# Optimization experiments

Hardware: AMD Instinct MI355X
Metric: run time of the kernel (lower is better)

## Reference

```python
import jax, jax.numpy as jnp
import numpy as np

T_ITERS = 48  # number of unrolled PDHG iterations (init kwarg T)


def _grad3(u):
    """Forward-difference gradient with circular BC.
    u: (P, 1, X, Y, T) -> (P, 3, X, Y, T).
    conv with kernel (0,-1,1) + circular pad == roll(v,-1,axis) - v."""
    v = u[:, 0]
    return jnp.stack([jnp.roll(v, -1, axis=a) - v for a in (1, 2, 3)], axis=1)


def _grad3_adj(q):
    """Adjoint (negative divergence) with circular BC.
    q: (P, 3, X, Y, T) -> (P, 1, X, Y, T)."""
    out = sum(jnp.roll(q[:, d], 1, axis=d + 1) - q[:, d] for d in range(3))
    return out[:, None]


def setup_inputs() -> dict:
    key = jax.random.key(0)
    k1, k2 = jax.random.split(key)
    x = jax.random.normal(k1, (2, 1, 160, 160, 16), dtype=jnp.float32)
    # positive per-voxel regularization map, one per gradient direction
    lambda_map = jax.random.uniform(k2, (2, 3, 160, 160, 16), dtype=jnp.float32)
    return {"x": x, "lambda_map": lambda_map}


def reference(x, lambda_map):
    # op_norm_AHA = 1, op_norm_GHG = sqrt(12) -> L = sqrt(1 + 12)
    L = jnp.sqrt(jnp.asarray(13.0, x.dtype))
    s10 = jax.nn.sigmoid(jnp.asarray(10.0, x.dtype))  # sigmoid of init value 10.0
    sigma = s10 / L
    tau = s10 / L
    theta = s10

    xnoisy = x
    p = x
    q = jnp.zeros((x.shape[0], 3) + x.shape[2:], dtype=x.dtype)
    x0 = x
    xbar = x

    def step(carry, _):
        p, q, x0, xbar = carry
        p = (p + sigma * (xbar - xnoisy)) / (1.0 + sigma)
        q = jnp.clip(q + sigma * _grad3(xbar), -lambda_map, lambda_map)
        x1 = x0 - tau * p - tau * _grad3_adj(q)
        xbar = x1 + theta * (x1 - x0)
        return (p, q, x1, xbar), None

    (p, q, x1, xbar), _ = jax.lax.scan(step, (p, q, x0, xbar), None, length=T_ITERS)
    return x1
```

## Files before the change

kernel.cpp:

```cpp
#include <hip/hip_runtime.h>
#include <math.h>

#define XDIM 160
#define YDIM 160
#define TDIM 16
#define NB 2
#define T_ITERS 48
#define TILE 10
#define R1S 16
#define R0S 18
#define TPT (XDIM / TILE)

constexpr int VOL  = XDIM * YDIM * TDIM;
constexpr int NX   = NB * VOL;
constexpr int NBLK = NB * TPT * TPT;

typedef _Float16 hreal;
typedef _Float16 half4 __attribute__((ext_vector_type(4)));

__device__ __forceinline__ float clampl(float v, float l) {
    return fminf(fmaxf(v, -l), l);
}
__device__ __forceinline__ int wrap(int v) {
    return v < 0 ? v + XDIM : (v >= XDIM ? v - XDIM : v);
}
__device__ __forceinline__ void ld4(const float* p, float* d) {
    float4 v = *(const float4*)p;
    d[0] = v.x; d[1] = v.y; d[2] = v.z; d[3] = v.w;
}
__device__ __forceinline__ void st4(float* p, const float* s) {
    *(float4*)p = make_float4(s[0], s[1], s[2], s[3]);
}
__device__ __forceinline__ void h2f4(const hreal* p, float* d) {
    half4 v = *(const half4*)p;
    d[0] = (float)v.x; d[1] = (float)v.y; d[2] = (float)v.z; d[3] = (float)v.w;
}

__global__ __launch_bounds__(256) void init_kernel(
    const float* __restrict__ x, const float* __restrict__ lam,
    float* __restrict__ pA, float* __restrict__ xA,
    hreal* __restrict__ xbAh, hreal* __restrict__ qAh,
    hreal* __restrict__ lamh, hreal* __restrict__ xnh)
{
    int i = blockIdx.x * blockDim.x + threadIdx.x;
    if (i < NX) {
        float v = x[i];
        pA[i] = v; xA[i] = v;
        xbAh[i] = (hreal)v;
        xnh[i]  = (hreal)v;
    }
    if (i < 3 * NX) {
        qAh[i]  = (hreal)0.f;
        lamh[i] = (hreal)lam[i];
    }
}

__global__ __launch_bounds__(256, 2) void pd_step4(
    const hreal* __restrict__ xnh, const hreal* __restrict__ lamh,
    const float* __restrict__ pIn, float* __restrict__ pOut,
    const float* __restrict__ xIn, float* __restrict__ xOut,
    const hreal* __restrict__ xbIn, hreal* __restrict__ xbOut,
    const hreal* __restrict__ qIn, hreal* __restrict__ qOut,
    float sigma, float inv1ps, float tau, float theta)
{
    __shared__ float xbS[R0S * R0S * TDIM];
    __shared__ float q0S[(R1S + 1) * R1S * TDIM];
    __shared__ float q1S[R1S * (R1S + 1) * TDIM];

    const int tid = threadIdx.x;
    const int b   = blockIdx.x / (TPT * TPT);
    const int rem = blockIdx.x % (TPT * TPT);
    const int X0  = (rem / TPT) * TILE;
    const int Y0  = (rem % TPT) * TILE;
    const int xbase = b * VOL, qbase = b * 3 * VOL;

    const int qd = tid & 3, t0 = qd * 4;
    const int lane  = tid & 63;
    const int upSrc = (lane & 60) | ((lane + 1) & 3);
    const int dnSrc = (lane & 60) | ((lane + 3) & 3);

    for (int s = tid; s < R0S * R0S * 4; s += 256) {
        int sq = s & 3, ln = s >> 2;
        int rx = ln / R0S, ry = ln % R0S;
        int gx = wrap(X0 - 4 + rx), gy = wrap(Y0 - 4 + ry);
        float v[4];
        h2f4(xbIn + xbase + (gx * YDIM + gy) * TDIM + sq * 4, v);
        st4(xbS + ln * TDIM + sq * 4, v);
    }
    for (int s = tid; s < 17 * 16 * 4; s += 256) {
        int sq = s & 3, ln = s >> 2;
        int sx = ln / 16, sy = ln % 16;
        int gx = wrap(X0 - 4 + sx), gy = wrap(Y0 - 3 + sy);
        float v[4];
        h2f4(qIn + qbase + (gx * YDIM + gy) * TDIM + sq * 4, v);
        st4(q0S + ln * TDIM + sq * 4, v);
    }
    for (int s = tid; s < 16 * 17 * 4; s += 256) {
        int sq = s & 3, ln = s >> 2;
        int sx = ln / 17, sy = ln % 17;
        int gx = wrap(X0 - 3 + sx), gy = wrap(Y0 - 4 + sy);
        float v[4];
        h2f4(qIn + qbase + VOL + (gx * YDIM + gy) * TDIM + sq * 4, v);
        st4(q1S + ln * TDIM + sq * 4, v);
    }

    float p[4][4], xv[4][4], xb[4][4], q0[4][4], q1[4][4], q2[4][4];
    half4 XNr[4], L0r[4], L1r[4], L2r[4];
    #pragma unroll
    for (int m = 0; m < 4; ++m) {
        int line = 64 * m + (tid >> 2);
        int lx = line >> 4, ly = line & 15;
        int gx = wrap(X0 - 3 + lx), gy = wrap(Y0 - 3 + ly);
        int off  = xbase + (gx * YDIM + gy) * TDIM + t0;
        int qoff = qbase + (gx * YDIM + gy) * TDIM + t0;
        ld4(pIn + off, p[m]);
        ld4(xIn + off, xv[m]);
        h2f4(xbIn + off, xb[m]);
        h2f4(qIn + qoff + 2 * VOL, q2[m]);
        XNr[m] = *(const half4*)(xnh + off);
        L0r[m] = *(const half4*)(lamh + qoff);
        L1r[m] = *(const half4*)(lamh + qoff + VOL);
        L2r[m] = *(const half4*)(lamh + qoff + 2 * VOL);
    }

    half4 LRr;
    if (tid < 64) {
        int rly = tid >> 2;
        LRr = *(const half4*)(lamh + qbase +
              (wrap(X0 - 4) * YDIM + wrap(Y0 - 3 + rly)) * TDIM + t0);
    } else if (tid < 128) {
        int rlx = (tid - 64) >> 2;
        LRr = *(const half4*)(lamh + qbase + VOL +
              (wrap(X0 - 3 + rlx) * YDIM + wrap(Y0 - 4)) * TDIM + t0);
    }

    __syncthreads();

    #pragma unroll
    for (int k = 1; k <= 4; ++k) {
        const int lo = k - 1, hi = 17 - k;

        if (k == 1) {
            if (tid < 64) {
                int rly = tid >> 2;
                float qr[4], xbc[4], xpx[4];
                ld4(q0S + (0 * R1S + rly) * TDIM + t0, qr);
                ld4(xbS + (0 * R0S + (rly + 1)) * TDIM + t0, xbc);
                ld4(xbS + (1 * R0S + (rly + 1)) * TDIM + t0, xpx);
                #pragma unroll
                for (int j = 0; j < 4; ++j)
                    qr[j] = clampl(qr[j] + sigma * (xpx[j] - xbc[j]), (float)LRr[j]);
                st4(q0S + (0 * R1S + rly) * TDIM + t0, qr);
            } else if (tid < 128) {
                int rlx = (tid - 64) >> 2;
                float qr[4], xbc[4], xpy[4];
                ld4(q1S + (rlx * 17 + 0) * TDIM + t0, qr);
                ld4(xbS + ((rlx + 1) * R0S + 0) * TDIM + t0, xbc);
                ld4(xbS + ((rlx + 1) * R0S + 1) * TDIM + t0, xpy);
                #pragma unroll
                for (int j = 0; j < 4; ++j)
                    qr[j] = clampl(qr[j] + sigma * (xpy[j] - xbc[j]), (float)LRr[j]);
                st4(q1S + (rlx * 17 + 0) * TDIM + t0, qr);
            }
        }

        #pragma unroll
        for (int m = 0; m < 4; ++m) {
            int line = 64 * m + (tid >> 2);
            int lx = line >> 4, ly = line & 15;
            bool inX = (lx >= lo && lx < hi), inY = (ly >= lo && ly < hi);
            bool aq0 = inY && (lx >= lo - 1) && (lx < hi);
            bool aq1 = inX && (ly >= lo - 1) && (ly < hi);
            bool ax  = inX && inY;

            if (k == 1) {
                ld4(q0S + ((lx + 1) * R1S + ly) * TDIM + t0, q0[m]);
                ld4(q1S + (lx * 17 + (ly + 1)) * TDIM + t0, q1[m]);
            }
            if (aq0) {
                float xpx[4];
                ld4(xbS + ((lx + 2) * R0S + (ly + 1)) * TDIM + t0, xpx);
                #pragma unroll
                for (int j = 0; j < 4; ++j)
                    q0[m][j] = clampl(q0[m][j] + sigma * (xpx[j] - xb[m][j]),
                                      (float)L0r[m][j]);
                st4(q0S + ((lx + 1) * R1S + ly) * TDIM + t0, q0[m]);
            }
            if (aq1) {
                float xpy[4];
                ld4(xbS + ((lx + 1) * R0S + (ly + 2)) * TDIM + t0, xpy);
                #pragma unroll
                for (int j = 0; j < 4; ++j)
                    q1[m][j] = clampl(q1[m][j] + sigma * (xpy[j] - xb[m][j]),
                                      (float)L1r[m][j]);
                st4(q1S + (lx * 17 + (ly + 1)) * TDIM + t0, q1[m]);
            }
            if (ax) {
                float xb_tp = __shfl(xb[m][0], upSrc, 64);
                #pragma unroll
                for (int j = 0; j < 4; ++j) {
                    float gt = ((j < 3) ? xb[m][j + 1] : xb_tp) - xb[m][j];
                    q2[m][j] = clampl(q2[m][j] + sigma * gt, (float)L2r[m][j]);
                    p[m][j]  = (p[m][j] + sigma * (xb[m][j] - (float)XNr[m][j]))
                               * inv1ps;
                }
            }
        }
        __syncthreads();

        #pragma unroll
        for (int m = 0; m < 4; ++m) {
            int line = 64 * m + (tid >> 2);
            int lx = line >> 4, ly = line & 15;
            bool ax = (lx >= lo && lx < hi && ly >= lo && ly < hi);
            if (ax) {
                float q0b[4], q1b[4];
                ld4(q0S + (lx * R1S + ly) * TDIM + t0, q0b);
                ld4(q1S + (lx * 17 + ly) * TDIM + t0, q1b);
                float q2tm = __shfl(q2[m][3], dnSrc, 64);
                #pragma unroll
                for (int j = 0; j < 4; ++j) {
                    float q2p = (j == 0) ? q2tm : q2[m][j - 1];
                    float div = (q0b[j] - q0[m][j]) + (q1b[j] - q1[m][j])
                              + (q2p - q2[m][j]);
                    float xnew = xv[m][j] - tau * (p[m][j] + div);
                    xb[m][j] = xnew + theta * (xnew - xv[m][j]);
                    xv[m][j] = xnew;
                }
                if (k < 4)
                    st4(xbS + ((lx + 1) * R0S + (ly + 1)) * TDIM + t0, xb[m]);
            }
        }
        if (k < 4) __syncthreads();
    }

    #pragma unroll
    for (int m = 0; m < 4; ++m) {
        int line = 64 * m + (tid >> 2);
        int lx = line >> 4, ly = line & 15;
        if (lx >= 3 && lx < 13 && ly >= 3 && ly < 13) {
            int gx = X0 + lx - 3, gy = Y0 + ly - 3;
            int off  = xbase + (gx * YDIM + gy) * TDIM + t0;
            int qoff = qbase + (gx * YDIM + gy) * TDIM + t0;
            st4(pOut + off, p[m]);
            st4(xOut + off, xv[m]);
            half4 h;
            h.x = (hreal)xb[m][0]; h.y = (hreal)xb[m][1];
            h.z = (hreal)xb[m][2]; h.w = (hreal)xb[m][3];
            *(half4*)(xbOut + off) = h;
            h.x = (hreal)q0[m][0]; h.y = (hreal)q0[m][1];
            h.z = (hreal)q0[m][2]; h.w = (hreal)q0[m][3];
            *(half4*)(qOut + qoff) = h;
            h.x = (hreal)q1[m][0]; h.y = (hreal)q1[m][1];
            h.z = (hreal)q1[m][2]; h.w = (hreal)q1[m][3];
            *(half4*)(qOut + qoff + VOL) = h;
            h.x = (hreal)q2[m][0]; h.y = (hreal)q2[m][1];
            h.z = (hreal)q2[m][2]; h.w = (hreal)q2[m][3];
            *(half4*)(qOut + qoff + 2 * VOL) = h;
        }
    }
}

extern "C" void kernel_launch(void* const* d_in, const int* in_sizes, int n_in,
                              void* d_out, int out_size, void* d_ws, size_t ws_size,
                              hipStream_t stream) {
    const float* x   = (const float*)d_in[0];
    const float* lam = (const float*)d_in[1];
    float* out = (float*)d_out;
    float* ws  = (float*)d_ws;

    float* pA  = ws;
    float* pB  = ws + (size_t)NX;
    float* xBb = ws + (size_t)2 * NX;
    float* xAb = out;
    hreal* hb  = (hreal*)(ws + (size_t)3 * NX);
    hreal* xbAh = hb;
    hreal* xbBh = hb + (size_t)NX;
    hreal* qAh  = hb + (size_t)2 * NX;
    hreal* qBh  = hb + (size_t)5 * NX;
    hreal* lamh = hb + (size_t)8 * NX;
    hreal* xnh  = hb + (size_t)11 * NX;

    const double s10 = 1.0 / (1.0 + exp(-10.0));
    const double L   = sqrt(13.0);
    float sigma  = (float)(s10 / L);
    float tau    = sigma;
    float theta  = (float)s10;
    float inv1ps = (float)(1.0 / (1.0 + s10 / L));

    init_kernel<<<(3 * NX + 255) / 256, 256, 0, stream>>>(
        x, lam, pA, xAb, xbAh, qAh, lamh, xnh);

    for (int j = 0; j < T_ITERS / 4; ++j) {
        const bool e = (j & 1) == 0;
        pd_step4<<<NBLK, 256, 0, stream>>>(
            xnh, lamh,
            e ? pA : pB,   e ? pB : pA,
            e ? xAb : xBb, e ? xBb : xAb,
            e ? xbAh : xbBh, e ? xbBh : xbAh,
            e ? qAh : qBh,  e ? qBh : qAh,
            sigma, inv1ps, tau, theta);
    }
}
```

Before: 298.3 us.

## Fuse eight PDHG iterations per launch with fp16 shared-memory tiles

```diff
diff --git a/kernel.cpp b/kernel.cpp
--- a/kernel.cpp
+++ b/kernel.cpp
@@ -7,9 +7,12 @@
 #define NB 2
 #define T_ITERS 48
 #define TILE 10
-#define R1S 16
-#define R0S 18
+#define KFUSE 8
+#define S1 24
+#define S0 26
 #define TPT (XDIM / TILE)
+#define NTHR 512
+#define NSLOT 5
 
 constexpr int VOL  = XDIM * YDIM * TDIM;
 constexpr int NX   = NB * VOL;
@@ -34,6 +37,11 @@
 __device__ __forceinline__ void h2f4(const hreal* p, float* d) {
     half4 v = *(const half4*)p;
     d[0] = (float)v.x; d[1] = (float)v.y; d[2] = (float)v.z; d[3] = (float)v.w;
+}
+__device__ __forceinline__ void f2h4(hreal* p, const float* s) {
+    half4 v;
+    v.x = (hreal)s[0]; v.y = (hreal)s[1]; v.z = (hreal)s[2]; v.w = (hreal)s[3];
+    *(half4*)p = v;
 }
 
 __global__ __launch_bounds__(256) void init_kernel(
@@ -55,7 +63,7 @@
     }
 }
 
-__global__ __launch_bounds__(256, 2) void pd_step4(
+__global__ __launch_bounds__(NTHR, 4) void pd_step8(
     const hreal* __restrict__ xnh, const hreal* __restrict__ lamh,
     const float* __restrict__ pIn, float* __restrict__ pOut,
     const float* __restrict__ xIn, float* __restrict__ xOut,
@@ -63,9 +71,9 @@
     const hreal* __restrict__ qIn, hreal* __restrict__ qOut,
     float sigma, float inv1ps, float tau, float theta)
 {
-    __shared__ float xbS[R0S * R0S * TDIM];
-    __shared__ float q0S[(R1S + 1) * R1S * TDIM];
-    __shared__ float q1S[R1S * (R1S + 1) * TDIM];
+    __shared__ __align__(16) hreal xbS[S0 * S0 * TDIM];
+    __shared__ __align__(16) hreal q0S[(S1 + 1) * S1 * TDIM];
+    __shared__ __align__(16) hreal q1S[S1 * (S1 + 1) * TDIM];
 
     const int tid = threadIdx.x;
     const int b   = blockIdx.x / (TPT * TPT);
@@ -74,134 +82,133 @@
     const int Y0  = (rem % TPT) * TILE;
     const int xbase = b * VOL, qbase = b * 3 * VOL;
 
-    const int qd = tid & 3, t0 = qd * 4;
+    const int t0 = (tid & 3) * 4;
     const int lane  = tid & 63;
     const int upSrc = (lane & 60) | ((lane + 1) & 3);
     const int dnSrc = (lane & 60) | ((lane + 3) & 3);
 
-    for (int s = tid; s < R0S * R0S * 4; s += 256) {
+    for (int s = tid; s < S0 * S0 * 4; s += NTHR) {
         int sq = s & 3, ln = s >> 2;
-        int rx = ln / R0S, ry = ln % R0S;
-        int gx = wrap(X0 - 4 + rx), gy = wrap(Y0 - 4 + ry);
-        float v[4];
-        h2f4(xbIn + xbase + (gx * YDIM + gy) * TDIM + sq * 4, v);
-        st4(xbS + ln * TDIM + sq * 4, v);
-    }
-    for (int s = tid; s < 17 * 16 * 4; s += 256) {
+        int rx = ln / S0, ry = ln % S0;
+        int gx = wrap(X0 - 8 + rx), gy = wrap(Y0 - 8 + ry);
+        *(half4*)(xbS + ln * TDIM + sq * 4) =
+            *(const half4*)(xbIn + xbase + (gx * YDIM + gy) * TDIM + sq * 4);
+    }
+    for (int s = tid; s < (S1 + 1) * S1 * 4; s += NTHR) {
         int sq = s & 3, ln = s >> 2;
-        int sx = ln / 16, sy = ln % 16;
-        int gx = wrap(X0 - 4 + sx), gy = wrap(Y0 - 3 + sy);
-        float v[4];
-        h2f4(qIn + qbase + (gx * YDIM + gy) * TDIM + sq * 4, v);
-        st4(q0S + ln * TDIM + sq * 4, v);
-    }
-    for (int s = tid; s < 16 * 17 * 4; s += 256) {
+        int sx = ln / S1, sy = ln % S1;
+        int gx = wrap(X0 - 8 + sx), gy = wrap(Y0 - 7 + sy);
+        *(half4*)(q0S + ln * TDIM + sq * 4) =
+            *(const half4*)(qIn + qbase + (gx * YDIM + gy) * TDIM + sq * 4);
+    }
+    for (int s = tid; s < S1 * (S1 + 1) * 4; s += NTHR) {
         int sq = s & 3, ln = s >> 2;
-        int sx = ln / 17, sy = ln % 17;
-        int gx = wrap(X0 - 3 + sx), gy = wrap(Y0 - 4 + sy);
-        float v[4];
-        h2f4(qIn + qbase + VOL + (gx * YDIM + gy) * TDIM + sq * 4, v);
-        st4(q1S + ln * TDIM + sq * 4, v);
-    }
-
-    float p[4][4], xv[4][4], xb[4][4], q0[4][4], q1[4][4], q2[4][4];
-    half4 XNr[4], L0r[4], L1r[4], L2r[4];
+        int sx = ln / (S1 + 1), sy = ln % (S1 + 1);
+        int gx = wrap(X0 - 7 + sx), gy = wrap(Y0 - 8 + sy);
+        *(half4*)(q1S + ln * TDIM + sq * 4) =
+            *(const half4*)(qIn + qbase + VOL + (gx * YDIM + gy) * TDIM + sq * 4);
+    }
+
+    float p[NSLOT][4], xv[NSLOT][4], q2[NSLOT][4];
+    half4 XNr[NSLOT], L0r[NSLOT], L1r[NSLOT], L2r[NSLOT];
     #pragma unroll
-    for (int m = 0; m < 4; ++m) {
-        int line = 64 * m + (tid >> 2);
-        int lx = line >> 4, ly = line & 15;
-        int gx = wrap(X0 - 3 + lx), gy = wrap(Y0 - 3 + ly);
-        int off  = xbase + (gx * YDIM + gy) * TDIM + t0;
-        int qoff = qbase + (gx * YDIM + gy) * TDIM + t0;
-        ld4(pIn + off, p[m]);
-        ld4(xIn + off, xv[m]);
-        h2f4(xbIn + off, xb[m]);
-        h2f4(qIn + qoff + 2 * VOL, q2[m]);
-        XNr[m] = *(const half4*)(xnh + off);
-        L0r[m] = *(const half4*)(lamh + qoff);
-        L1r[m] = *(const half4*)(lamh + qoff + VOL);
-        L2r[m] = *(const half4*)(lamh + qoff + 2 * VOL);
+    for (int m = 0; m < NSLOT; ++m) {
+        int line = m * (NTHR / 4) + (tid >> 2);
+        if (line < S1 * S1) {
+            int lx = line / S1, ly = line % S1;
+            int gx = wrap(X0 - (KFUSE - 1) + lx), gy = wrap(Y0 - (KFUSE - 1) + ly);
+            int off  = xbase + (gx * YDIM + gy) * TDIM + t0;
+            int qoff = qbase + (gx * YDIM + gy) * TDIM + t0;
+            ld4(pIn + off, p[m]);
+            ld4(xIn + off, xv[m]);
+            h2f4(qIn + qoff + 2 * VOL, q2[m]);
+            XNr[m] = *(const half4*)(xnh + off);
+            L0r[m] = *(const half4*)(lamh + qoff);
+            L1r[m] = *(const half4*)(lamh + qoff + VOL);
+            L2r[m] = *(const half4*)(lamh + qoff + 2 * VOL);
+        }
     }
 
     half4 LRr;
-    if (tid < 64) {
+    if (tid < S1 * 4) {
         int rly = tid >> 2;
         LRr = *(const half4*)(lamh + qbase +
-              (wrap(X0 - 4) * YDIM + wrap(Y0 - 3 + rly)) * TDIM + t0);
-    } else if (tid < 128) {
-        int rlx = (tid - 64) >> 2;
+              (wrap(X0 - 8) * YDIM + wrap(Y0 - 7 + rly)) * TDIM + t0);
+    } else if (tid < 2 * S1 * 4) {
+        int rlx = (tid - S1 * 4) >> 2;
         LRr = *(const half4*)(lamh + qbase + VOL +
-              (wrap(X0 - 3 + rlx) * YDIM + wrap(Y0 - 4)) * TDIM + t0);
+              (wrap(X0 - 7 + rlx) * YDIM + wrap(Y0 - 8)) * TDIM + t0);
     }
 
     __syncthreads();
 
-    #pragma unroll
-    for (int k = 1; k <= 4; ++k) {
-        const int lo = k - 1, hi = 17 - k;
+    for (int k = 1; k <= KFUSE; ++k) {
+        const int lo = k - 1, hi = S1 + 1 - k;
 
         if (k == 1) {
-            if (tid < 64) {
+            if (tid < S1 * 4) {
                 int rly = tid >> 2;
                 float qr[4], xbc[4], xpx[4];
-                ld4(q0S + (0 * R1S + rly) * TDIM + t0, qr);
-                ld4(xbS + (0 * R0S + (rly + 1)) * TDIM + t0, xbc);
-                ld4(xbS + (1 * R0S + (rly + 1)) * TDIM + t0, xpx);
+                h2f4(q0S + (0 * S1 + rly) * TDIM + t0, qr);
+                h2f4(xbS + (0 * S0 + (rly + 1)) * TDIM + t0, xbc);
+                h2f4(xbS + (1 * S0 + (rly + 1)) * TDIM + t0, xpx);
                 #pragma unroll
                 for (int j = 0; j < 4; ++j)
                     qr[j] = clampl(qr[j] + sigma * (xpx[j] - xbc[j]), (float)LRr[j]);
-                st4(q0S + (0 * R1S + rly) * TDIM + t0, qr);
-            } else if (tid < 128) {
-                int rlx = (tid - 64) >> 2;
+                f2h4(q0S + (0 * S1 + rly) * TDIM + t0, qr);
+            } else if (tid < 2 * S1 * 4) {
+                int rlx = (tid - S1 * 4) >> 2;
                 float qr[4], xbc[4], xpy[4];
-                ld4(q1S + (rlx * 17 + 0) * TDIM + t0, qr);
-                ld4(xbS + ((rlx + 1) * R0S + 0) * TDIM + t0, xbc);
-                ld4(xbS + ((rlx + 1) * R0S + 1) * TDIM + t0, xpy);
+                h2f4(q1S + (rlx * (S1 + 1) + 0) * TDIM + t0, qr);
+                h2f4(xbS + ((rlx + 1) * S0 + 0) * TDIM + t0, xbc);
+                h2f4(xbS + ((rlx + 1) * S0 + 1) * TDIM + t0, xpy);
                 #pragma unroll
                 for (int j = 0; j < 4; ++j)
                     qr[j] = clampl(qr[j] + sigma * (xpy[j] - xbc[j]), (float)LRr[j]);
-                st4(q1S + (rlx * 17 + 0) * TDIM + t0, qr);
+                f2h4(q1S + (rlx * (S1 + 1) + 0) * TDIM + t0, qr);
             }
         }
 
         #pragma unroll
-        for (int m = 0; m < 4; ++m) {
-            int line = 64 * m + (tid >> 2);
-            int lx = line >> 4, ly = line & 15;
-            bool inX = (lx >= lo && lx < hi), inY = (ly >= lo && ly < hi);
-            bool aq0 = inY && (lx >= lo - 1) && (lx < hi);
-            bool aq1 = inX && (ly >= lo - 1) && (ly < hi);
-            bool ax  = inX && inY;
-
-            if (k == 1) {
-                ld4(q0S + ((lx + 1) * R1S + ly) * TDIM + t0, q0[m]);
-                ld4(q1S + (lx * 17 + (ly + 1)) * TDIM + t0, q1[m]);
-            }
+        for (int m = 0; m < NSLOT; ++m) {
+            int line = m * (NTHR / 4) + (tid >> 2);
+            bool act = line < S1 * S1;
+            int lx = act ? line / S1 : 0, ly = act ? line % S1 : 0;
+            bool inX = lx >= lo && lx < hi, inY = ly >= lo && ly < hi;
+            bool aq0 = act && inY && (lx >= lo - 1) && (lx < hi);
+            bool aq1 = act && inX && (ly >= lo - 1) && (ly < hi);
+            bool ax  = act && inX && inY;
+
+            float xbo[4];
+            h2f4(xbS + ((lx + 1) * S0 + (ly + 1)) * TDIM + t0, xbo);
+
             if (aq0) {
-                float xpx[4];
-                ld4(xbS + ((lx + 2) * R0S + (ly + 1)) * TDIM + t0, xpx);
+                float xpx[4], qv[4];
+                h2f4(xbS + ((lx + 2) * S0 + (ly + 1)) * TDIM + t0, xpx);
+                h2f4(q0S + ((lx + 1) * S1 + ly) * TDIM + t0, qv);
                 #pragma unroll
                 for (int j = 0; j < 4; ++j)
-                    q0[m][j] = clampl(q0[m][j] + sigma * (xpx[j] - xb[m][j]),
-                                      (float)L0r[m][j]);
-                st4(q0S + ((lx + 1) * R1S + ly) * TDIM + t0, q0[m]);
+                    qv[j] = clampl(qv[j] + sigma * (xpx[j] - xbo[j]),
+                                   (float)L0r[m][j]);
+                f2h4(q0S + ((lx + 1) * S1 + ly) * TDIM + t0, qv);
             }
             if (aq1) {
-                float xpy[4];
-                ld4(xbS + ((lx + 1) * R0S + (ly + 2)) * TDIM + t0, xpy);
+                float xpy[4], qv[4];
+                h2f4(xbS + ((lx + 1) * S0 + (ly + 2)) * TDIM + t0, xpy);
+                h2f4(q1S + (lx * (S1 + 1) + (ly + 1)) * TDIM + t0, qv);
                 #pragma unroll
                 for (int j = 0; j < 4; ++j)
-                    q1[m][j] = clampl(q1[m][j] + sigma * (xpy[j] - xb[m][j]),
-                                      (float)L1r[m][j]);
-                st4(q1S + (lx * 17 + (ly + 1)) * TDIM + t0, q1[m]);
+                    qv[j] = clampl(qv[j] + sigma * (xpy[j] - xbo[j]),
+                                   (float)L1r[m][j]);
+                f2h4(q1S + (lx * (S1 + 1) + (ly + 1)) * TDIM + t0, qv);
             }
             if (ax) {
-                float xb_tp = __shfl(xb[m][0], upSrc, 64);
+                float xb_tp = __shfl(xbo[0], upSrc, 64);
                 #pragma unroll
                 for (int j = 0; j < 4; ++j) {
-                    float gt = ((j < 3) ? xb[m][j + 1] : xb_tp) - xb[m][j];
+                    float gt = ((j < 3) ? xbo[j + 1] : xb_tp) - xbo[j];
                     q2[m][j] = clampl(q2[m][j] + sigma * gt, (float)L2r[m][j]);
-                    p[m][j]  = (p[m][j] + sigma * (xb[m][j] - (float)XNr[m][j]))
+                    p[m][j]  = (p[m][j] + sigma * (xbo[j] - (float)XNr[m][j]))
                                * inv1ps;
                 }
             }
@@ -209,55 +216,46 @@
         __syncthreads();
 
         #pragma unroll
-        for (int m = 0; m < 4; ++m) {
-            int line = 64 * m + (tid >> 2);
-            int lx = line >> 4, ly = line & 15;
-            bool ax = (lx >= lo && lx < hi && ly >= lo && ly < hi);
+        for (int m = 0; m < NSLOT; ++m) {
+            int line = m * (NTHR / 4) + (tid >> 2);
+            bool act = line < S1 * S1;
+            int lx = act ? line / S1 : 0, ly = act ? line % S1 : 0;
+            bool ax = act && lx >= lo && lx < hi && ly >= lo && ly < hi;
+
+            float q2tm = __shfl(q2[m][3], dnSrc, 64);
             if (ax) {
-                float q0b[4], q1b[4];
-                ld4(q0S + (lx * R1S + ly) * TDIM + t0, q0b);
-                ld4(q1S + (lx * 17 + ly) * TDIM + t0, q1b);
-                float q2tm = __shfl(q2[m][3], dnSrc, 64);
+                float q0o[4], q0b[4], q1o[4], q1b[4];
+                h2f4(q0S + ((lx + 1) * S1 + ly) * TDIM + t0, q0o);
+                h2f4(q0S + (lx * S1 + ly) * TDIM + t0, q0b);
+                h2f4(q1S + (lx * (S1 + 1) + (ly + 1)) * TDIM + t0, q1o);
+                h2f4(q1S + (lx * (S1 + 1) + ly) * TDIM + t0, q1b);
+
+                float xbn[4];
                 #pragma unroll
                 for (int j = 0; j < 4; ++j) {
                     float q2p = (j == 0) ? q2tm : q2[m][j - 1];
-                    float div = (q0b[j] - q0[m][j]) + (q1b[j] - q1[m][j])
+                    float div = (q0b[j] - q0o[j]) + (q1b[j] - q1o[j])
                               + (q2p - q2[m][j]);
                     float xnew = xv[m][j] - tau * (p[m][j] + div);
-                    xb[m][j] = xnew + theta * (xnew - xv[m][j]);
+                    xbn[j] = xnew + theta * (xnew - xv[m][j]);
                     xv[m][j] = xnew;
                 }
-                if (k < 4)
-                    st4(xbS + ((lx + 1) * R0S + (ly + 1)) * TDIM + t0, xb[m]);
+                if (k < KFUSE) {
+                    f2h4(xbS + ((lx + 1) * S0 + (ly + 1)) * TDIM + t0, xbn);
+                } else {
+                    int gx = X0 + lx - (KFUSE - 1), gy = Y0 + ly - (KFUSE - 1);
+                    int off  = xbase + (gx * YDIM + gy) * TDIM + t0;
+                    int qoff = qbase + (gx * YDIM + gy) * TDIM + t0;
+                    st4(pOut + off, p[m]);
+                    st4(xOut + off, xv[m]);
+                    f2h4(xbOut + off, xbn);
+                    f2h4(qOut + qoff, q0o);
+                    f2h4(qOut + qoff + VOL, q1o);
+                    f2h4(qOut + qoff + 2 * VOL, q2[m]);
+                }
             }
         }
-        if (k < 4) __syncthreads();
-    }
-
-    #pragma unroll
-    for (int m = 0; m < 4; ++m) {
-        int line = 64 * m + (tid >> 2);
-        int lx = line >> 4, ly = line & 15;
-        if (lx >= 3 && lx < 13 && ly >= 3 && ly < 13) {
-            int gx = X0 + lx - 3, gy = Y0 + ly - 3;
-            int off  = xbase + (gx * YDIM + gy) * TDIM + t0;
-            int qoff = qbase + (gx * YDIM + gy) * TDIM + t0;
-            st4(pOut + off, p[m]);
-            st4(xOut + off, xv[m]);
-            half4 h;
-            h.x = (hreal)xb[m][0]; h.y = (hreal)xb[m][1];
-            h.z = (hreal)xb[m][2]; h.w = (hreal)xb[m][3];
-            *(half4*)(xbOut + off) = h;
-            h.x = (hreal)q0[m][0]; h.y = (hreal)q0[m][1];
-            h.z = (hreal)q0[m][2]; h.w = (hreal)q0[m][3];
-            *(half4*)(qOut + qoff) = h;
-            h.x = (hreal)q1[m][0]; h.y = (hreal)q1[m][1];
-            h.z = (hreal)q1[m][2]; h.w = (hreal)q1[m][3];
-            *(half4*)(qOut + qoff + VOL) = h;
-            h.x = (hreal)q2[m][0]; h.y = (hreal)q2[m][1];
-            h.z = (hreal)q2[m][2]; h.w = (hreal)q2[m][3];
-            *(half4*)(qOut + qoff + 2 * VOL) = h;
-        }
+        if (k < KFUSE) __syncthreads();
     }
 }
 
@@ -291,9 +289,9 @@
     init_kernel<<<(3 * NX + 255) / 256, 256, 0, stream>>>(
         x, lam, pA, xAb, xbAh, qAh, lamh, xnh);
 
-    for (int j = 0; j < T_ITERS / 4; ++j) {
+    for (int j = 0; j < T_ITERS / KFUSE; ++j) {
         const bool e = (j & 1) == 0;
-        pd_step4<<<NBLK, 256, 0, stream>>>(
+        pd_step8<<<NBLK, NTHR, 0, stream>>>(
             xnh, lamh,
             e ? pA : pB,   e ? pB : pA,
             e ? xAb : xBb, e ? xBb : xAb,
```

Result: slower. 1.141 ms (+282.3%).
